# Performance work log

Hardware: AMD Instinct MI355X
Metric: run time of the kernel (lower is better)

The kernel has to match this reference:

```python
import jax, jax.numpy as jnp
import numpy as np

H = 1024  # hidden_dim
DT = 0.1
LN_EPS = 1e-5


def setup_inputs() -> dict:
    key = jax.random.key(0)
    ks = jax.random.split(key, 8)
    h = H
    ph = h // 2
    x = jax.random.normal(ks[0], (8, 2048, h), dtype=jnp.float32)
    # S initialized to identity in torch; add small noise so math is non-trivial
    S = jnp.eye(h, dtype=jnp.float32) + 0.02 * jax.random.normal(ks[1], (h, h), dtype=jnp.float32)
    # Hamiltonian MLP: Linear(h,h) -> tanh -> Linear(h,1)
    lim1 = 1.0 / np.sqrt(h)
    W1 = jax.random.uniform(ks[2], (h, h), minval=-lim1, maxval=lim1, dtype=jnp.float32)
    b1 = jax.random.uniform(ks[3], (h,), minval=-lim1, maxval=lim1, dtype=jnp.float32)
    w2 = jax.random.uniform(ks[4], (h,), minval=-lim1, maxval=lim1, dtype=jnp.float32)
    b2 = jax.random.uniform(ks[5], (1,), minval=-lim1, maxval=lim1, dtype=jnp.float32)
    # symplectic structure matrix J (buffer)
    I = jnp.eye(ph, dtype=jnp.float32)
    J = jnp.zeros((h, h), dtype=jnp.float32)
    J = J.at[:ph, ph:].set(I)
    J = J.at[ph:, :ph].set(-I)
    gamma = jnp.ones((h,), dtype=jnp.float32)
    beta = jnp.zeros((h,), dtype=jnp.float32)
    return {"x": x, "S": S, "W1": W1, "b1": b1, "w2": w2, "b2": b2,
            "J": J, "gamma": gamma, "beta": beta, "num_steps": 3}


def reference(x, S, W1, b1, w2, b2, J, gamma, beta, num_steps):
    h = x.shape[-1]
    # Cayley-approx symplectic projection (training branch): S_sym = I + 2*A, A skew part
    A = (S - S.T) * 0.5
    S_sym = jnp.eye(h, dtype=x.dtype) + 2.0 * A
    # z = einsum('ij,...j->...i', S_sym, x)
    z = x @ S_sym.T
    for _ in range(num_steps):
        # analytic grad of H(z) = w2 . tanh(z W1^T + b1) + b2 wrt z
        t = jnp.tanh(z @ W1.T + b1)             # [..., h]
        grad_H = ((1.0 - t * t) * w2) @ W1       # [..., h]
        flow = grad_H @ J.T                      # einsum('ij,...j->...i', J, grad_H)
        z = z + DT * flow
    y = z + x
    # LayerNorm over last dim
    mu = jnp.mean(y, axis=-1, keepdims=True)
    var = jnp.mean((y - mu) ** 2, axis=-1, keepdims=True)
    return (y - mu) * jax.lax.rsqrt(var + LN_EPS) * gamma + beta
```

## Files before the change

### kernel.cpp

```cpp
#include <hip/hip_runtime.h>
#include <hip/hip_bf16.h>

#define H 1024
#define PH 512
#define MROWS 16384
#define DT 0.1f
#define LN_EPS 1e-5f

#define BM 128
#define BN 128
#define BK 64

typedef short s16x8 __attribute__((ext_vector_type(8)));
typedef float f32x4 __attribute__((ext_vector_type(4)));

__device__ __forceinline__ float b2f(short v) {
    union { float f; unsigned u; } c;
    c.u = ((unsigned)(unsigned short)v) << 16;
    return c.f;
}
__device__ __forceinline__ short f2b(float f) {
    union { float f; unsigned u; } c;
    c.f = f;
    unsigned u = c.u;
    unsigned r = u + 0x7FFFu + ((u >> 16) & 1u);
    return (short)(r >> 16);
}
__device__ __forceinline__ float ftanh(float s) {
    float e = __expf(2.0f * s);
    return 1.0f - 2.0f * __builtin_amdgcn_rcpf(e + 1.0f);
}

__global__ __launch_bounds__(256)
void prep_ab(const float* __restrict__ S, const float* __restrict__ W1,
             short* __restrict__ Wsym, short* __restrict__ W1b,
             short* __restrict__ Wflow, short* __restrict__ WflowT) {
    int idx = blockIdx.x * 256 + threadIdx.x;
    int i = idx >> 10, j = idx & 1023;
    Wsym[idx] = f2b(S[i * H + j] - S[j * H + i]);
    W1b[idx]  = f2b(W1[idx]);
    int p = (i + PH) & (H - 1);
    short w = f2b(W1[j * H + p]);
    if (i >= PH) w ^= (short)0x8000;
    Wflow[idx] = w;
    int q = (j + PH) & (H - 1);
    short wt = f2b(W1[i * H + q]);
    if (j >= PH) wt ^= (short)0x8000;
    WflowT[idx] = wt;
}

__global__ __launch_bounds__(256)
void cvt_x(const float* __restrict__ x, short* __restrict__ xb) {
    int t = blockIdx.x * 256 + threadIdx.x;
    const float4* p = (const float4*)x + (size_t)t * 2;
    float4 f0 = p[0], f1 = p[1];
    s16x8 v;
    v[0] = f2b(f0.x); v[1] = f2b(f0.y); v[2] = f2b(f0.z); v[3] = f2b(f0.w);
    v[4] = f2b(f1.x); v[5] = f2b(f1.y); v[6] = f2b(f1.z); v[7] = f2b(f1.w);
    ((s16x8*)xb)[t] = v;
}

template <int KIND, bool G2D>
__global__ __launch_bounds__(256, 4)
void gemm_k(const short* __restrict__ A, const short* __restrict__ Bw,
            short* __restrict__ out,
            const float* __restrict__ xf,
            const float* __restrict__ w2f,
            const short* __restrict__ u0r,
            const short* __restrict__ pg,
            short* __restrict__ out2,
            float clampv)
{
    __shared__ short As[BM * BK];
    __shared__ short Bs[BN * BK];

    const int tid  = threadIdx.x;
    const int lane = tid & 63;
    const int wave = tid >> 6;
    const int wm   = wave >> 1;
    const int wn   = wave & 1;

    int m0, n0;
    if (G2D) {
        m0 = blockIdx.y * BM;
        n0 = blockIdx.x * BN;
    } else {
        const int lid   = blockIdx.x;
        const int chunk = ((lid & 7) << 7) | (lid >> 3);
        m0 = (chunk >> 3) * BM;
        n0 = (chunk & 7) * BN;
    }

    const int lrow = lane & 15;
    const int quad = lane >> 4;
    const int swzr = (lrow & 7) << 4;

    const int srow  = lane >> 3;
    const int selem = 8 * ((lane & 7) ^ srow);

    f32x4 acc[4][4] = {};

    for (int k0 = 0; k0 < H; k0 += BK) {
#pragma unroll
        for (int i = 0; i < 4; ++i) {
            int ch = wave * 4 + i;
            const short* asrc = A  + (size_t)(m0 + ch * 8 + srow) * H + k0 + selem;
            const short* bsrc = Bw + (size_t)(n0 + ch * 8 + srow) * H + k0 + selem;
            __builtin_amdgcn_global_load_lds(
                (const __attribute__((address_space(1))) void*)asrc,
                (__attribute__((address_space(3))) void*)(As + ch * 512), 16, 0, 0);
            __builtin_amdgcn_global_load_lds(
                (const __attribute__((address_space(1))) void*)bsrc,
                (__attribute__((address_space(3))) void*)(Bs + ch * 512), 16, 0, 0);
        }
        __syncthreads();

#pragma unroll
        for (int ks = 0; ks < 2; ++ks) {
            s16x8 af[4], bfr[4];
#pragma unroll
            for (int mt = 0; mt < 4; ++mt) {
                int row = wm * 64 + mt * 16 + lrow;
                af[mt] = *(const s16x8*)((const char*)As + row * 128 +
                                         ((ks * 64 + quad * 16) ^ swzr));
            }
#pragma unroll
            for (int nt = 0; nt < 4; ++nt) {
                int col = wn * 64 + nt * 16 + lrow;
                bfr[nt] = *(const s16x8*)((const char*)Bs + col * 128 +
                                          ((ks * 64 + quad * 16) ^ swzr));
            }
#pragma unroll
            for (int mt = 0; mt < 4; ++mt)
#pragma unroll
                for (int nt = 0; nt < 4; ++nt)
                    acc[mt][nt] = __builtin_amdgcn_mfma_f32_16x16x32_bf16(
                        bfr[nt], af[mt], acc[mt][nt], 0, 0, 0);
        }
        __syncthreads();
    }

    float4 bvv[4], wvv[4];
    if (KIND == 1 || KIND == 3 || KIND == 4) {
#pragma unroll
        for (int nt = 0; nt < 4; ++nt) {
            int col = n0 + wn * 64 + nt * 16 + quad * 4;
            bvv[nt] = *(const float4*)(xf + col);
            wvv[nt] = *(const float4*)(w2f + col);
        }
    }
#pragma unroll
    for (int mt = 0; mt < 4; ++mt) {
        const int row = m0 + wm * 64 + mt * 16 + lrow;
        const size_t rbase = (size_t)row * H;
#pragma unroll
        for (int nt = 0; nt < 4; ++nt) {
            const int col = n0 + wn * 64 + nt * 16 + quad * 4;
            const size_t idx = rbase + col;
            f32x4 a = acc[mt][nt];
            short4 o;
            if (KIND == 0) {
                float4 xv = *(const float4*)(xf + idx);
                o.x = f2b(a[0] + xv.x);
                o.y = f2b(a[1] + xv.y);
                o.z = f2b(a[2] + xv.z);
                o.w = f2b(a[3] + xv.w);
                *(short4*)(out + idx) = o;
            } else if (KIND == 1) {
                float t0 = ftanh(a[0] + bvv[nt].x);
                float t1 = ftanh(a[1] + bvv[nt].y);
                float t2 = ftanh(a[2] + bvv[nt].z);
                float t3 = ftanh(a[3] + bvv[nt].w);
                o.x = f2b((1.0f - t0 * t0) * wvv[nt].x);
                o.y = f2b((1.0f - t1 * t1) * wvv[nt].y);
                o.z = f2b((1.0f - t2 * t2) * wvv[nt].z);
                o.w = f2b((1.0f - t3 * t3) * wvv[nt].w);
                *(short4*)(out + idx) = o;
            } else if (KIND == 2) {
                short4 zo = *(const short4*)(out + idx);
                float d0 = fminf(fmaxf(DT * a[0], -clampv), clampv);
                float d1 = fminf(fmaxf(DT * a[1], -clampv), clampv);
                float d2 = fminf(fmaxf(DT * a[2], -clampv), clampv);
                float d3 = fminf(fmaxf(DT * a[3], -clampv), clampv);
                o.x = f2b(b2f(zo.x) + d0);
                o.y = f2b(b2f(zo.y) + d1);
                o.z = f2b(b2f(zo.z) + d2);
                o.w = f2b(b2f(zo.w) + d3);
                *(short4*)(out + idx) = o;
            } else if (KIND == 3) {
                short4 u;
                u.x = f2b(a[0]); u.y = f2b(a[1]); u.z = f2b(a[2]); u.w = f2b(a[3]);
                *(short4*)(out + idx) = u;
                float t0 = ftanh(a[0] + bvv[nt].x);
                float t1 = ftanh(a[1] + bvv[nt].y);
                float t2 = ftanh(a[2] + bvv[nt].z);
                float t3 = ftanh(a[3] + bvv[nt].w);
                o.x = f2b((1.0f - t0 * t0) * wvv[nt].x);
                o.y = f2b((1.0f - t1 * t1) * wvv[nt].y);
                o.z = f2b((1.0f - t2 * t2) * wvv[nt].z);
                o.w = f2b((1.0f - t3 * t3) * wvv[nt].w);
                *(short4*)(out2 + idx) = o;
            } else if (KIND == 4) {
                short4 u4 = *(const short4*)(u0r + idx);
                short4 p4 = *(const short4*)(pg + idx);
                float t0 = ftanh(b2f(u4.x) + a[0] + bvv[nt].x);
                float t1 = ftanh(b2f(u4.y) + a[1] + bvv[nt].y);
                float t2 = ftanh(b2f(u4.z) + a[2] + bvv[nt].z);
                float t3 = ftanh(b2f(u4.w) + a[3] + bvv[nt].w);
                o.x = f2b(b2f(p4.x) + (1.0f - t0 * t0) * wvv[nt].x);
                o.y = f2b(b2f(p4.y) + (1.0f - t1 * t1) * wvv[nt].y);
                o.z = f2b(b2f(p4.z) + (1.0f - t2 * t2) * wvv[nt].z);
                o.w = f2b(b2f(p4.w) + (1.0f - t3 * t3) * wvv[nt].w);
                *(short4*)(out2 + idx) = o;
            } else {
                o.x = f2b(DT * a[0]);
                o.y = f2b(DT * a[1]);
                o.z = f2b(DT * a[2]);
                o.w = f2b(DT * a[3]);
                *(short4*)(out + idx) = o;
            }
        }
    }
}

__global__ __launch_bounds__(256)
void ln_k(const short* __restrict__ z, const float* __restrict__ x,
          const float* __restrict__ gamma, const float* __restrict__ beta,
          float* __restrict__ out) {
    const int row = blockIdx.x;
    const int tid = threadIdx.x;
    const size_t base = (size_t)row * H;
    short4 z4 = ((const short4*)(z + base))[tid];
    float4 x4 = ((const float4*)(x + base))[tid];
    float y0 = b2f(z4.x) + x4.x;
    float y1 = b2f(z4.y) + x4.y;
    float y2 = b2f(z4.z) + x4.z;
    float y3 = b2f(z4.w) + x4.w;
    float s = y0 + y1 + y2 + y3;
    float q = y0 * y0 + y1 * y1 + y2 * y2 + y3 * y3;
#pragma unroll
    for (int off = 32; off > 0; off >>= 1) {
        s += __shfl_down(s, off);
        q += __shfl_down(q, off);
    }
    __shared__ float ss[4], qs[4];
    if ((tid & 63) == 0) { ss[tid >> 6] = s; qs[tid >> 6] = q; }
    __syncthreads();
    s = ss[0] + ss[1] + ss[2] + ss[3];
    q = qs[0] + qs[1] + qs[2] + qs[3];
    const float mu  = s * (1.0f / H);
    const float var = q * (1.0f / H) - mu * mu;
    const float rs  = rsqrtf(var + LN_EPS);
    const int col = tid * 4;
    float4 o;
    o.x = (y0 - mu) * rs * gamma[col + 0] + beta[col + 0];
    o.y = (y1 - mu) * rs * gamma[col + 1] + beta[col + 1];
    o.z = (y2 - mu) * rs * gamma[col + 2] + beta[col + 2];
    o.w = (y3 - mu) * rs * gamma[col + 3] + beta[col + 3];
    ((float4*)(out + base))[tid] = o;
}

extern "C" void kernel_launch(void* const* d_in, const int* in_sizes, int n_in,
                              void* d_out, int out_size, void* d_ws, size_t ws_size,
                              hipStream_t stream) {
    int ix = 0;
    for (int i = 0; i < n_in; ++i)
        if (in_sizes[i] == MROWS * H) { ix = i; break; }

    const float *x, *S, *W1, *b1, *w2, *gamma, *beta;
    if (ix == 0) {
        x     = (const float*)d_in[0];
        S     = (const float*)d_in[1];
        W1    = (const float*)d_in[2];
        b1    = (const float*)d_in[3];
        w2    = (const float*)d_in[4];
        gamma = (const float*)d_in[7];
        beta  = (const float*)d_in[8];
    } else {
        S     = (const float*)d_in[1];
        W1    = (const float*)d_in[2];
        b1    = (const float*)d_in[3];
        beta  = (const float*)d_in[5];
        gamma = (const float*)d_in[6];
        w2    = (const float*)d_in[8];
        x     = (const float*)d_in[ix];
    }

    const size_t MB = 1024 * 1024;
    float* out    = (float*)d_out;
    short* xb     = (short*)d_out;
    short* u0     = (short*)d_out;
    char*  hi     = (char*)d_out + 32 * MB;
    short* Wsym   = (short*)(hi);
    short* W1b    = (short*)(hi + 2 * MB);
    short* Wflow  = (short*)(hi + 4 * MB);
    short* WflowT = (short*)(hi + 6 * MB);
    short* GT     = (short*)(hi + 8 * MB);
    short* z      = (short*)d_ws;
    short* gsumA  = (short*)((char*)d_ws + 32 * MB);
    short* gsumB  = (short*)((char*)d_ws + 64 * MB);

    const bool fast = ws_size >= 96 * MB;

    prep_ab<<<(H * H) / 256, 256, 0, stream>>>(S, W1, Wsym, W1b, Wflow, WflowT);
    cvt_x  <<<(MROWS * H / 8) / 256, 256, 0, stream>>>(x, xb);

    const int nblk = (H / BN) * (MROWS / BM);
    if (fast) {
        gemm_k<5, true><<<dim3(H / BN, H / BM), 256, 0, stream>>>(
            W1b, WflowT, GT, nullptr, nullptr, nullptr, nullptr, nullptr, 0.0f);
        gemm_k<0, false><<<nblk, 256, 0, stream>>>(
            xb, Wsym, z, x, nullptr, nullptr, nullptr, nullptr, 0.0f);
        gemm_k<3, false><<<nblk, 256, 0, stream>>>(
            z, W1b, u0, b1, w2, nullptr, nullptr, gsumA, 0.0f);
        gemm_k<4, false><<<nblk, 256, 0, stream>>>(
            gsumA, GT, nullptr, b1, w2, u0, gsumA, gsumB, 0.0f);
        gemm_k<4, false><<<nblk, 256, 0, stream>>>(
            gsumB, GT, nullptr, b1, w2, u0, gsumB, gsumA, 0.0f);
        gemm_k<2, false><<<nblk, 256, 0, stream>>>(
            gsumA, Wflow, z, nullptr, nullptr, nullptr, nullptr, nullptr, 0.03f);
    } else {
        short* g = (short*)d_out;
        gemm_k<0, false><<<nblk, 256, 0, stream>>>(
            xb, Wsym, z, x, nullptr, nullptr, nullptr, nullptr, 0.0f);
        for (int step = 0; step < 3; ++step) {
            gemm_k<1, false><<<nblk, 256, 0, stream>>>(
                z, W1b, g, b1, w2, nullptr, nullptr, nullptr, 0.0f);
            gemm_k<2, false><<<nblk, 256, 0, stream>>>(
                g, Wflow, z, nullptr, nullptr, nullptr, nullptr, nullptr, 0.01f);
        }
    }
    ln_k<<<MROWS, 256, 0, stream>>>(z, x, gamma, beta, out);
}
```

Baseline: 424.0 us.

## Double-buffer GEMM LDS tiles and tile-transpose weight prep kernel

The GEMM main loop now uses two LDS buffers: it issues the async global-to-LDS loads for the next K tile, then waits only on the older loads with a partial vmcnt before computing on the current tile. This overlaps memory latency with MFMA work. It doubles LDS use per block and lowers the occupancy hint from 4 to 2 blocks. The weight prep kernel is also rewritten to do its transposes through shared-memory tiles, so the strided global reads and writes of the old version become coalesced.

```diff
diff --git a/kernel.cpp b/kernel.cpp
--- a/kernel.cpp
+++ b/kernel.cpp
@@ -32,21 +32,40 @@
 }
 
 __global__ __launch_bounds__(256)
-void prep_ab(const float* __restrict__ S, const float* __restrict__ W1,
-             short* __restrict__ Wsym, short* __restrict__ W1b,
-             short* __restrict__ Wflow, short* __restrict__ WflowT) {
-    int idx = blockIdx.x * 256 + threadIdx.x;
-    int i = idx >> 10, j = idx & 1023;
-    Wsym[idx] = f2b(S[i * H + j] - S[j * H + i]);
-    W1b[idx]  = f2b(W1[idx]);
-    int p = (i + PH) & (H - 1);
-    short w = f2b(W1[j * H + p]);
-    if (i >= PH) w ^= (short)0x8000;
-    Wflow[idx] = w;
-    int q = (j + PH) & (H - 1);
-    short wt = f2b(W1[i * H + q]);
-    if (j >= PH) wt ^= (short)0x8000;
-    WflowT[idx] = wt;
+void prep_t(const float* __restrict__ S, const float* __restrict__ W1,
+            short* __restrict__ Wsym, short* __restrict__ W1b,
+            short* __restrict__ Wflow, short* __restrict__ WflowT) {
+    __shared__ float T0[64][65];
+    __shared__ float T1[64][65];
+    __shared__ short Ts[64][66];
+    const int I = blockIdx.y * 64, J = blockIdx.x * 64;
+    const int c  = threadIdx.x & 63;
+    const int r0 = (threadIdx.x >> 6) * 16;
+#pragma unroll
+    for (int rr = 0; rr < 16; ++rr) {
+        int r = r0 + rr;
+        T0[r][c] = S[(size_t)(I + r) * H + J + c];
+        T1[r][c] = S[(size_t)(J + r) * H + I + c];
+    }
+    __syncthreads();
+    const int pJ = (J + PH) & (H - 1);
+    const short sflip = (J >= PH) ? (short)0x8000 : (short)0;
+#pragma unroll
+    for (int rr = 0; rr < 16; ++rr) {
+        int r = r0 + rr;
+        size_t rowb = (size_t)(I + r) * H;
+        Wsym[rowb + J + c] = f2b(T0[r][c] - T1[c][r]);
+        W1b [rowb + J + c] = f2b(W1[rowb + J + c]);
+        short wt = (short)(f2b(W1[rowb + pJ + c]) ^ sflip);
+        WflowT[rowb + J + c] = wt;
+        Ts[r][c] = wt;
+    }
+    __syncthreads();
+#pragma unroll
+    for (int rr = 0; rr < 16; ++rr) {
+        int r = r0 + rr;
+        Wflow[(size_t)(J + r) * H + I + c] = Ts[c][r];
+    }
 }
 
 __global__ __launch_bounds__(256)
@@ -61,7 +80,7 @@
 }
 
 template <int KIND, bool G2D>
-__global__ __launch_bounds__(256, 4)
+__global__ __launch_bounds__(256, 2)
 void gemm_k(const short* __restrict__ A, const short* __restrict__ Bw,
             short* __restrict__ out,
             const float* __restrict__ xf,
@@ -71,8 +90,8 @@
             short* __restrict__ out2,
             float clampv)
 {
-    __shared__ short As[BM * BK];
-    __shared__ short Bs[BN * BK];
+    __shared__ short As[2][BM * BK];
+    __shared__ short Bs[2][BN * BK];
 
     const int tid  = threadIdx.x;
     const int lane = tid & 63;
@@ -100,7 +119,7 @@
 
     f32x4 acc[4][4] = {};
 
-    for (int k0 = 0; k0 < H; k0 += BK) {
+    auto STAGE = [&](int sel, int k0) {
 #pragma unroll
         for (int i = 0; i < 4; ++i) {
             int ch = wave * 4 + i;
@@ -108,26 +127,26 @@
             const short* bsrc = Bw + (size_t)(n0 + ch * 8 + srow) * H + k0 + selem;
             __builtin_amdgcn_global_load_lds(
                 (const __attribute__((address_space(1))) void*)asrc,
-                (__attribute__((address_space(3))) void*)(As + ch * 512), 16, 0, 0);
+                (__attribute__((address_space(3))) void*)(&As[sel][ch * 512]), 16, 0, 0);
             __builtin_amdgcn_global_load_lds(
                 (const __attribute__((address_space(1))) void*)bsrc,
-                (__attribute__((address_space(3))) void*)(Bs + ch * 512), 16, 0, 0);
-        }
-        __syncthreads();
-
+                (__attribute__((address_space(3))) void*)(&Bs[sel][ch * 512]), 16, 0, 0);
+        }
+    };
+    auto COMPUTE = [&](int sel) {
 #pragma unroll
         for (int ks = 0; ks < 2; ++ks) {
             s16x8 af[4], bfr[4];
 #pragma unroll
             for (int mt = 0; mt < 4; ++mt) {
                 int row = wm * 64 + mt * 16 + lrow;
-                af[mt] = *(const s16x8*)((const char*)As + row * 128 +
+                af[mt] = *(const s16x8*)((const char*)&As[sel][0] + row * 128 +
                                          ((ks * 64 + quad * 16) ^ swzr));
             }
 #pragma unroll
             for (int nt = 0; nt < 4; ++nt) {
                 int col = wn * 64 + nt * 16 + lrow;
-                bfr[nt] = *(const s16x8*)((const char*)Bs + col * 128 +
+                bfr[nt] = *(const s16x8*)((const char*)&Bs[sel][0] + col * 128 +
                                           ((ks * 64 + quad * 16) ^ swzr));
             }
 #pragma unroll
@@ -137,8 +156,21 @@
                     acc[mt][nt] = __builtin_amdgcn_mfma_f32_16x16x32_bf16(
                         bfr[nt], af[mt], acc[mt][nt], 0, 0, 0);
         }
-        __syncthreads();
-    }
+    };
+
+    STAGE(0, 0);
+    int cur = 0;
+    for (int t = 0; t < (H / BK) - 1; ++t) {
+        STAGE(cur ^ 1, (t + 1) * BK);
+        asm volatile("s_waitcnt vmcnt(8)" ::: "memory");
+        __builtin_amdgcn_s_barrier();
+        COMPUTE(cur);
+        __builtin_amdgcn_s_barrier();
+        cur ^= 1;
+    }
+    asm volatile("s_waitcnt vmcnt(0)" ::: "memory");
+    __builtin_amdgcn_s_barrier();
+    COMPUTE(cur);
 
     float4 bvv[4], wvv[4];
     if (KIND == 1 || KIND == 3 || KIND == 4) {
@@ -302,8 +334,8 @@
 
     const bool fast = ws_size >= 96 * MB;
 
-    prep_ab<<<(H * H) / 256, 256, 0, stream>>>(S, W1, Wsym, W1b, Wflow, WflowT);
-    cvt_x  <<<(MROWS * H / 8) / 256, 256, 0, stream>>>(x, xb);
+    prep_t<<<dim3(16, 16), 256, 0, stream>>>(S, W1, Wsym, W1b, Wflow, WflowT);
+    cvt_x <<<(MROWS * H / 8) / 256, 256, 0, stream>>>(x, xb);
 
     const int nblk = (H / BN) * (MROWS / BM);
     if (fast) {
```

Result: no change. 426.6 us (+0.6%).
